# Optimization experiments

Measured on AMD Instinct MI355X. Metric: run time of the kernel, lower is better.

The kernel has to match this reference:

```python
import jax, jax.numpy as jnp
import numpy as np

D = 1024          # d_model
E = 12            # n_routed
HS = 2 * D        # shared hidden (r_shared=2)
HR = 3 * D        # routed hidden (r_routed=3)
TAU = 1.5         # router temperature


def setup_inputs() -> dict:
    key = jax.random.key(0)
    ks = jax.random.split(key, 12)
    def xavier(k, shape):
        fan_in, fan_out = shape[-2], shape[-1]
        lim = jnp.sqrt(6.0 / (fan_in + fan_out))
        return jax.random.uniform(k, shape, jnp.float32, -lim, lim)
    x = jax.random.normal(ks[0], (2, 1024, D), jnp.float32)
    # shared expert (n_shared=1, GEGLU)
    Ws1 = xavier(ks[1], (D, 2 * HS)); bs1 = jnp.zeros((2 * HS,), jnp.float32)
    Ws2 = xavier(ks[2], (HS, D));     bs2 = jnp.zeros((D,), jnp.float32)
    # routed experts, stacked [E, ...]
    We1 = xavier(ks[3], (E, D, 2 * HR)); be1 = jnp.zeros((E, 2 * HR), jnp.float32)
    We2 = xavier(ks[4], (E, HR, D));     be2 = jnp.zeros((E, D), jnp.float32)
    # router
    Wr = xavier(ks[5], (D, E)); br = jnp.zeros((E,), jnp.float32)
    return {"x": x, "Ws1": Ws1, "bs1": bs1, "Ws2": Ws2, "bs2": bs2,
            "We1": We1, "be1": be1, "We2": We2, "be2": be2, "Wr": Wr, "br": br}


def _geglu(h):
    a, g = jnp.split(h, 2, axis=-1)
    return a * jax.nn.gelu(g, approximate=False)  # torch GELU is exact erf


def reference(x, Ws1, bs1, Ws2, bs2, We1, be1, We2, be2, Wr, br):
    B, T, Dm = x.shape
    xf = x.reshape(-1, Dm)                                   # [N, D]
    # shared expert (n_shared=1 -> divide by 1)
    ys = _geglu(xf @ Ws1 + bs1) @ Ws2 + bs2                  # [N, D]
    # top-2 router (eval: no noise)
    logits = (xf @ Wr + br) / TAU                            # [N, E]
    top_val, top_idx = jax.lax.top_k(logits, 2)              # [N, 2]
    top_w = jax.nn.softmax(top_val, axis=-1)                 # [N, 2]
    # combine weights per (token, expert); non-selected experts get 0
    onehot = jax.nn.one_hot(top_idx, E, dtype=x.dtype)       # [N, 2, E]
    w = jnp.einsum('nke,nk->ne', onehot, top_w)              # [N, E]
    # dropless dense dispatch: every expert sees all tokens, weight 0 masks
    h = jnp.einsum('nd,edh->enh', xf, We1) + be1[:, None, :] # [E, N, 2*HR]
    act = _geglu(h)                                          # [E, N, HR]
    yE = jnp.einsum('enh,ehd->end', act, We2) + be2[:, None, :]
    yr = jnp.einsum('end,ne->nd', yE, w)                     # [N, D]
    return (ys + yr).reshape(B, T, Dm)
```

## Files before the change

kernel.cpp:

```cpp
#include <hip/hip_runtime.h>

#define N_TOK 2048
#define DMODEL 1024
#define NEXP 12
#define HS_DIM 2048
#define HR_DIM 3072

typedef __attribute__((ext_vector_type(8))) short bf16x8;
typedef __attribute__((ext_vector_type(4))) float f32x4;

#define AS1 __attribute__((address_space(1)))
#define AS3 __attribute__((address_space(3)))

__device__ __forceinline__ void gl_lds16(const void* g, void* l) {
  __builtin_amdgcn_global_load_lds((const AS1 void*)g, (AS3 void*)l, 16, 0, 0);
}

__device__ __forceinline__ unsigned short f2bf(float x) {
  union { float f; unsigned int u; } v; v.f = x;
  unsigned int u = v.u;
  u += 0x7fff + ((u >> 16) & 1);
  return (unsigned short)(u >> 16);
}
__device__ __forceinline__ unsigned pack2(float a, float b) {
  return (unsigned)f2bf(a) | ((unsigned)f2bf(b) << 16);
}
__device__ __forceinline__ float gelu_exact(float x) {
  return 0.5f * x * (1.0f + erff(x * 0.70710678118654752f));
}


__global__ __launch_bounds__(256)
void convert_x_kernel(const float* __restrict__ X, unsigned short* __restrict__ XB) {
  const int idx = (blockIdx.x * 256 + threadIdx.x) * 8;
  float4 f0 = *(const float4*)(X + idx);
  float4 f1 = *(const float4*)(X + idx + 4);
  uint4 o;
  o.x = pack2(f0.x, f0.y); o.y = pack2(f0.z, f0.w);
  o.z = pack2(f1.x, f1.y); o.w = pack2(f1.z, f1.w);
  *(uint4*)(XB + idx) = o;
}

__global__ __launch_bounds__(256)
void tconv_kernel(const float* __restrict__ W, unsigned short* __restrict__ WT,
                  int K, int N) {
  const int n0 = blockIdx.x * 64;
  const int k0 = blockIdx.y * 64;
  const size_t bo = (size_t)blockIdx.z * K * N;
  __shared__ unsigned short Ts[64 * 72];
  const int t = threadIdx.x;
  const int k4 = (t >> 4) * 4, n4 = (t & 15) * 4;
  float4 rw[4];
#pragma unroll
  for (int i = 0; i < 4; ++i)
    rw[i] = *(const float4*)(W + bo + (size_t)(k0 + k4 + i) * N + n0 + n4);
#pragma unroll
  for (int j = 0; j < 4; ++j) {
    uint2 v;
    v.x = pack2(((const float*)&rw[0])[j], ((const float*)&rw[1])[j]);
    v.y = pack2(((const float*)&rw[2])[j], ((const float*)&rw[3])[j]);
    *(uint2*)&Ts[(n4 + j) * 72 + k4] = v;
  }
  __syncthreads();
  const int n = t >> 2, kc = (t & 3) * 16;
  uint4 v0 = *(const uint4*)&Ts[n * 72 + kc];
  uint4 v1 = *(const uint4*)&Ts[n * 72 + kc + 8];
  unsigned short* dst = WT + (size_t)blockIdx.z * N * K + (size_t)(n0 + n) * K + k0 + kc;
  *(uint4*)dst = v0;
  *(uint4*)(dst + 8) = v1;
}


__global__ void init_kernel(int* counts, int* cursors) {
  int t = threadIdx.x;
  if (t < NEXP) { counts[t] = 0; cursors[t] = 0; }
}

__global__ __launch_bounds__(256)
void router_kernel(const float* __restrict__ X, const float* __restrict__ Wr,
                   const float* __restrict__ br, int* __restrict__ top_e,
                   float* __restrict__ top_w, int* __restrict__ counts) {
  const int wv = threadIdx.x >> 6, lane = threadIdx.x & 63;
  const int n = blockIdx.x * 4 + wv;
  float a[NEXP];
#pragma unroll
  for (int e = 0; e < NEXP; ++e) a[e] = 0.f;
  for (int it = 0; it < DMODEL / 64; ++it) {
    int k = it * 64 + lane;
    float xv = X[(size_t)n * DMODEL + k];
    const float* wr = Wr + (size_t)k * NEXP;
#pragma unroll
    for (int e = 0; e < NEXP; ++e) a[e] += xv * wr[e];
  }
#pragma unroll
  for (int e = 0; e < NEXP; ++e)
    for (int o = 32; o > 0; o >>= 1) a[e] += __shfl_xor(a[e], o, 64);
  if (lane == 0) {
    float l[NEXP];
#pragma unroll
    for (int e = 0; e < NEXP; ++e) l[e] = (a[e] + br[e]) * (1.0f / 1.5f);
    int e0 = 0;
    for (int e = 1; e < NEXP; ++e) if (l[e] > l[e0]) e0 = e;
    int e1 = (e0 == 0) ? 1 : 0;
    for (int e = 0; e < NEXP; ++e) if (e != e0 && l[e] > l[e1]) e1 = e;
    float w0 = 1.f / (1.f + expf(l[e1] - l[e0]));
    top_e[n * 2 + 0] = e0; top_e[n * 2 + 1] = e1;
    top_w[n * 2 + 0] = w0; top_w[n * 2 + 1] = 1.f - w0;
    atomicAdd(&counts[e0], 1); atomicAdd(&counts[e1], 1);
  }
}

__global__ void scan_kernel(const int* __restrict__ counts, int* __restrict__ offs) {
  if (threadIdx.x == 0) {
    int s = 0;
    for (int e = 0; e < NEXP; ++e) { offs[e] = s; s += counts[e]; }
    offs[NEXP] = s;
  }
}

__global__ __launch_bounds__(256)
void fill_kernel(const int* __restrict__ top_e, const float* __restrict__ top_w,
                 const int* __restrict__ offs, int* __restrict__ cursors,
                 int* __restrict__ slot_tok, float* __restrict__ slot_w) {
  int n = blockIdx.x * 256 + threadIdx.x;
  if (n >= N_TOK) return;
#pragma unroll
  for (int j = 0; j < 2; ++j) {
    int e = top_e[n * 2 + j];
    int p = atomicAdd(&cursors[e], 1);
    int s = offs[e] + p;
    slot_tok[s] = n;
    slot_w[s] = top_w[n * 2 + j];
  }
}

__global__ __launch_bounds__(256, 2)
void gemm1_kernel(const unsigned short* __restrict__ XB,
                  const unsigned short* __restrict__ W1T,
                  const float* __restrict__ B1, unsigned short* __restrict__ ACT,
                  const int* __restrict__ slot_tok, const int* __restrict__ offs,
                  const int* __restrict__ counts, int H, int Mtot) {
  const int e = blockIdx.z;
  const int n0 = blockIdx.x * 128;
  const int m0 = blockIdx.y * 128;
  const int count = counts ? counts[e] : N_TOK;
  if (m0 >= count) return;
  const int off = offs ? offs[e] : 0;
  const unsigned short* W = W1T + (size_t)e * 2 * H * DMODEL;
  const float* bias = B1 + (size_t)e * 2 * H;

  __shared__ unsigned short As[128 * 32];
  __shared__ unsigned short Bs[256 * 32];

  const int t = threadIdx.x;
  const int lane = t & 63, wv = t >> 6;
  const int srow = t >> 2, skc = t & 3;

  int r0 = m0 + srow, r1 = m0 + srow + 64;
  if (slot_tok) {
    int s0 = off + r0; if (s0 >= Mtot) s0 = Mtot - 1;
    int s1 = off + r1; if (s1 >= Mtot) s1 = Mtot - 1;
    r0 = slot_tok[s0]; r1 = slot_tok[s1];
  }
  const unsigned short* ap0 = XB + (size_t)r0 * DMODEL + skc * 8;
  const unsigned short* ap1 = XB + (size_t)r1 * DMODEL + skc * 8;
  const unsigned short* bp[4];
#pragma unroll
  for (int ii = 0; ii < 4; ++ii) {
    int brow = srow + 64 * ii;
    int wrow = (brow < 128) ? (n0 + brow) : (H + n0 + brow - 128);
    bp[ii] = W + (size_t)wrow * DMODEL + skc * 8;
  }
  unsigned short* aL0 = &As[wv * 512];
  unsigned short* aL1 = &As[2048 + wv * 512];
  unsigned short* bL0 = &Bs[wv * 512];
  unsigned short* bL1 = &Bs[2048 + wv * 512];
  unsigned short* bL2 = &Bs[4096 + wv * 512];
  unsigned short* bL3 = &Bs[6144 + wv * 512];

  const int q = lane >> 4, rr = lane & 15;
  const int wr = wv >> 1, wc = wv & 1;

  f32x4 acc_a[4][4], acc_g[4][4];
#pragma unroll
  for (int i = 0; i < 4; ++i)
#pragma unroll
    for (int j = 0; j < 4; ++j) {
      acc_a[i][j] = (f32x4){0.f, 0.f, 0.f, 0.f};
      acc_g[i][j] = (f32x4){0.f, 0.f, 0.f, 0.f};
    }

  for (int kt = 0; kt < DMODEL / 32; ++kt) {
    const int kb = kt * 32;
    __syncthreads();
    gl_lds16(ap0 + kb, aL0);
    gl_lds16(ap1 + kb, aL1);
    gl_lds16(bp[0] + kb, bL0);
    gl_lds16(bp[1] + kb, bL1);
    gl_lds16(bp[2] + kb, bL2);
    gl_lds16(bp[3] + kb, bL3);
    __syncthreads();
    bf16x8 aF[4], bA[4], bG[4];
#pragma unroll
    for (int i = 0; i < 4; ++i)
      aF[i] = *(const bf16x8*)&As[(wr * 64 + i * 16 + rr) * 32 + q * 8];
#pragma unroll
    for (int j = 0; j < 4; ++j) {
      bA[j] = *(const bf16x8*)&Bs[(wc * 64 + j * 16 + rr) * 32 + q * 8];
      bG[j] = *(const bf16x8*)&Bs[(128 + wc * 64 + j * 16 + rr) * 32 + q * 8];
    }
#pragma unroll
    for (int i = 0; i < 4; ++i)
#pragma unroll
      for (int j = 0; j < 4; ++j) {
        acc_a[i][j] = __builtin_amdgcn_mfma_f32_16x16x32_bf16(aF[i], bA[j], acc_a[i][j], 0, 0, 0);
        acc_g[i][j] = __builtin_amdgcn_mfma_f32_16x16x32_bf16(aF[i], bG[j], acc_g[i][j], 0, 0, 0);
      }
  }

  float ba[4], bg[4];
#pragma unroll
  for (int j = 0; j < 4; ++j) {
    int col = wc * 64 + j * 16 + rr;
    ba[j] = bias[n0 + col];
    bg[j] = bias[H + n0 + col];
  }
#pragma unroll
  for (int i = 0; i < 4; ++i)
#pragma unroll
    for (int j = 0; j < 4; ++j)
#pragma unroll
      for (int reg = 0; reg < 4; ++reg) {
        int row = wr * 64 + i * 16 + q * 4 + reg;
        if (m0 + row < count) {
          int col = wc * 64 + j * 16 + rr;
          float av = acc_a[i][j][reg] + ba[j];
          float gv = acc_g[i][j][reg] + bg[j];
          ACT[(size_t)(off + m0 + row) * H + n0 + col] = f2bf(av * gelu_exact(gv));
        }
      }
}

__global__ __launch_bounds__(256, 2)
void gemm2_kernel(const unsigned short* __restrict__ ACT,
                  const unsigned short* __restrict__ W2T,
                  const float* __restrict__ B2, float* __restrict__ OUT,
                  const int* __restrict__ slot_tok, const float* __restrict__ slot_w,
                  const int* __restrict__ offs, const int* __restrict__ counts,
                  int K, int Mtot) {
  const int e = blockIdx.z;
  const int n0 = blockIdx.x * 128;
  const int m0 = blockIdx.y * 128;
  const int count = counts ? counts[e] : N_TOK;
  if (m0 >= count) return;
  const int off = offs ? offs[e] : 0;
  const unsigned short* W = W2T + (size_t)e * DMODEL * K;
  const float* bias = B2 + (size_t)e * DMODEL;

  __shared__ unsigned short As[128 * 32];
  __shared__ unsigned short Bs[128 * 32];

  const int t = threadIdx.x;
  const int lane = t & 63, wv = t >> 6;
  const int srow = t >> 2, skc = t & 3;

  int s0 = off + m0 + srow;      if (s0 >= Mtot) s0 = Mtot - 1;
  int s1 = off + m0 + srow + 64; if (s1 >= Mtot) s1 = Mtot - 1;
  const unsigned short* ap0 = ACT + (size_t)s0 * K + skc * 8;
  const unsigned short* ap1 = ACT + (size_t)s1 * K + skc * 8;
  const unsigned short* bp0 = W + (size_t)(n0 + srow) * K + skc * 8;
  const unsigned short* bp1 = W + (size_t)(n0 + srow + 64) * K + skc * 8;

  unsigned short* aL0 = &As[wv * 512];
  unsigned short* aL1 = &As[2048 + wv * 512];
  unsigned short* bL0 = &Bs[wv * 512];
  unsigned short* bL1 = &Bs[2048 + wv * 512];

  const int q = lane >> 4, rr = lane & 15;
  const int wr = wv >> 1, wc = wv & 1;

  f32x4 acc[4][4];
#pragma unroll
  for (int i = 0; i < 4; ++i)
#pragma unroll
    for (int j = 0; j < 4; ++j) acc[i][j] = (f32x4){0.f, 0.f, 0.f, 0.f};

  const int KT = K >> 5;
  for (int kt = 0; kt < KT; ++kt) {
    const int kb = kt * 32;
    __syncthreads();
    gl_lds16(ap0 + kb, aL0);
    gl_lds16(ap1 + kb, aL1);
    gl_lds16(bp0 + kb, bL0);
    gl_lds16(bp1 + kb, bL1);
    __syncthreads();
    bf16x8 aF[4], bF[4];
#pragma unroll
    for (int i = 0; i < 4; ++i)
      aF[i] = *(const bf16x8*)&As[(wr * 64 + i * 16 + rr) * 32 + q * 8];
#pragma unroll
    for (int j = 0; j < 4; ++j)
      bF[j] = *(const bf16x8*)&Bs[(wc * 64 + j * 16 + rr) * 32 + q * 8];
#pragma unroll
    for (int i = 0; i < 4; ++i)
#pragma unroll
      for (int j = 0; j < 4; ++j)
        acc[i][j] = __builtin_amdgcn_mfma_f32_16x16x32_bf16(aF[i], bF[j], acc[i][j], 0, 0, 0);
  }

  float bb[4];
#pragma unroll
  for (int j = 0; j < 4; ++j) bb[j] = bias[n0 + wc * 64 + j * 16 + rr];
#pragma unroll
  for (int i = 0; i < 4; ++i)
#pragma unroll
    for (int j = 0; j < 4; ++j)
#pragma unroll
      for (int reg = 0; reg < 4; ++reg) {
        int row = wr * 64 + i * 16 + q * 4 + reg;
        if (m0 + row < count) {
          int col = wc * 64 + j * 16 + rr;
          float v = acc[i][j][reg] + bb[j];
          if (slot_tok) {
            int s = off + m0 + row;
            atomicAdd(&OUT[(size_t)slot_tok[s] * DMODEL + n0 + col], slot_w[s] * v);
          } else {
            OUT[(size_t)(m0 + row) * DMODEL + n0 + col] = v;
          }
        }
      }
}


extern "C" void kernel_launch(void* const* d_in, const int* in_sizes, int n_in,
                              void* d_out, int out_size, void* d_ws, size_t ws_size,
                              hipStream_t stream) {
  const float* x   = (const float*)d_in[0];
  const float* Ws1 = (const float*)d_in[1];
  const float* bs1 = (const float*)d_in[2];
  const float* Ws2 = (const float*)d_in[3];
  const float* bs2 = (const float*)d_in[4];
  const float* We1 = (const float*)d_in[5];
  const float* be1 = (const float*)d_in[6];
  const float* We2 = (const float*)d_in[7];
  const float* be2 = (const float*)d_in[8];
  const float* Wr  = (const float*)d_in[9];
  const float* br  = (const float*)d_in[10];
  float* out = (float*)d_out;

  char* p = (char*)d_ws;
  int* counts  = (int*)p; p += 256;
  int* cursors = (int*)p; p += 256;
  int* offs    = (int*)p; p += 256;
  int* top_e   = (int*)p; p += (size_t)N_TOK * 2 * 4;
  float* top_w = (float*)p; p += (size_t)N_TOK * 2 * 4;
  int* slot_tok = (int*)p; p += (size_t)2 * N_TOK * 4;
  float* slot_w = (float*)p; p += (size_t)2 * N_TOK * 4;
  unsigned short* xb    = (unsigned short*)p; p += (size_t)N_TOK * DMODEL * 2;
  unsigned short* ws1t  = (unsigned short*)p; p += (size_t)2 * HS_DIM * DMODEL * 2;
  unsigned short* ws2t  = (unsigned short*)p; p += (size_t)DMODEL * HS_DIM * 2;
  unsigned short* we1t  = (unsigned short*)p; p += (size_t)NEXP * 2 * HR_DIM * DMODEL * 2;
  unsigned short* we2t  = (unsigned short*)p; p += (size_t)NEXP * DMODEL * HR_DIM * 2;
  unsigned short* act_s = (unsigned short*)p; p += (size_t)N_TOK * HS_DIM * 2;
  unsigned short* act_r = (unsigned short*)p; p += (size_t)2 * N_TOK * HR_DIM * 2;

  init_kernel<<<1, 64, 0, stream>>>(counts, cursors);
  router_kernel<<<N_TOK / 4, 256, 0, stream>>>(x, Wr, br, top_e, top_w, counts);
  scan_kernel<<<1, 64, 0, stream>>>(counts, offs);
  fill_kernel<<<N_TOK / 256, 256, 0, stream>>>(top_e, top_w, offs, cursors, slot_tok, slot_w);

  convert_x_kernel<<<(N_TOK * DMODEL) / 2048, 256, 0, stream>>>(x, xb);
  tconv_kernel<<<dim3(2 * HS_DIM / 64, DMODEL / 64, 1), 256, 0, stream>>>(Ws1, ws1t, DMODEL, 2 * HS_DIM);
  tconv_kernel<<<dim3(DMODEL / 64, HS_DIM / 64, 1), 256, 0, stream>>>(Ws2, ws2t, HS_DIM, DMODEL);
  tconv_kernel<<<dim3(2 * HR_DIM / 64, DMODEL / 64, NEXP), 256, 0, stream>>>(We1, we1t, DMODEL, 2 * HR_DIM);
  tconv_kernel<<<dim3(DMODEL / 64, HR_DIM / 64, NEXP), 256, 0, stream>>>(We2, we2t, HR_DIM, DMODEL);

  gemm1_kernel<<<dim3(HS_DIM / 128, N_TOK / 128, 1), 256, 0, stream>>>(
      xb, ws1t, bs1, act_s, nullptr, nullptr, nullptr, HS_DIM, N_TOK);
  gemm1_kernel<<<dim3(HR_DIM / 128, N_TOK / 128, NEXP), 256, 0, stream>>>(
      xb, we1t, be1, act_r, slot_tok, offs, counts, HR_DIM, 2 * N_TOK);

  gemm2_kernel<<<dim3(DMODEL / 128, N_TOK / 128, 1), 256, 0, stream>>>(
      act_s, ws2t, bs2, out, nullptr, nullptr, nullptr, nullptr, HS_DIM, N_TOK);
  gemm2_kernel<<<dim3(DMODEL / 128, N_TOK / 128, NEXP), 256, 0, stream>>>(
      act_r, we2t, be2, out, slot_tok, slot_w, offs, counts, HR_DIM, 2 * N_TOK);
}
```

Measured before the change: 1.030 ms.

## Merge shared and routed GEMMs into single launches with 32x32 MFMA and K=64 tiles

Combines the shared-expert and routed-expert GEMMs into one flat-grid launch per stage, so both sets of blocks can be scheduled together instead of running as separate serialized kernels. The compute moves from 16x16x32 to 32x32x16 bf16 MFMA and each K step loads 64 elements, which halves the number of barriers per tile and changes how fragments are reused. The output is now zeroed up front and the shared-expert result is written with atomics, which adds a zeroing pass and atomic traffic for the shared path. LDS use per block doubles, which may lower occupancy.

```diff
diff --git a/kernel.cpp b/kernel.cpp
--- a/kernel.cpp
+++ b/kernel.cpp
@@ -7,7 +7,7 @@
 #define HR_DIM 3072
 
 typedef __attribute__((ext_vector_type(8))) short bf16x8;
-typedef __attribute__((ext_vector_type(4))) float f32x4;
+typedef __attribute__((ext_vector_type(16))) float f32x16;
 
 #define AS1 __attribute__((address_space(1)))
 #define AS3 __attribute__((address_space(3)))
@@ -47,7 +47,7 @@
   const int n0 = blockIdx.x * 64;
   const int k0 = blockIdx.y * 64;
   const size_t bo = (size_t)blockIdx.z * K * N;
-  __shared__ unsigned short Ts[64 * 72];
+  __shared__ __align__(16) unsigned short Ts[64 * 72];
   const int t = threadIdx.x;
   const int k4 = (t >> 4) * 4, n4 = (t & 15) * 4;
   float4 rw[4];
@@ -134,198 +134,243 @@
   }
 }
 
+__global__ __launch_bounds__(256)
+void zero_out_kernel(float4* __restrict__ out) {
+  out[blockIdx.x * 256 + threadIdx.x] = make_float4(0.f, 0.f, 0.f, 0.f);
+}
+
+#define G1_SHARED 256
+#define G1_PER_E  384
+
 __global__ __launch_bounds__(256, 2)
-void gemm1_kernel(const unsigned short* __restrict__ XB,
-                  const unsigned short* __restrict__ W1T,
-                  const float* __restrict__ B1, unsigned short* __restrict__ ACT,
-                  const int* __restrict__ slot_tok, const int* __restrict__ offs,
-                  const int* __restrict__ counts, int H, int Mtot) {
-  const int e = blockIdx.z;
-  const int n0 = blockIdx.x * 128;
-  const int m0 = blockIdx.y * 128;
-  const int count = counts ? counts[e] : N_TOK;
+void gemm1_all_kernel(const unsigned short* __restrict__ XB,
+                      const unsigned short* __restrict__ WS,
+                      const unsigned short* __restrict__ WE,
+                      const float* __restrict__ BSb, const float* __restrict__ BEb,
+                      unsigned short* __restrict__ ACT_S, unsigned short* __restrict__ ACT_R,
+                      const int* __restrict__ slot_tok, const int* __restrict__ offs,
+                      const int* __restrict__ counts) {
+  int id = blockIdx.x;
+  const unsigned short* W; const float* bias; unsigned short* ACT;
+  int H, count, off, m0, n0, routed;
+  if (id < G1_SHARED) {
+    routed = 0;
+    m0 = (id >> 4) * 128; n0 = (id & 15) * 128;
+    W = WS; bias = BSb; ACT = ACT_S; H = HS_DIM; count = N_TOK; off = 0;
+  } else {
+    routed = 1;
+    id -= G1_SHARED;
+    const int e = id / G1_PER_E, rem = id % G1_PER_E;
+    m0 = (rem / 24) * 128; n0 = (rem % 24) * 128;
+    W = WE + (size_t)e * 2 * HR_DIM * DMODEL;
+    bias = BEb + (size_t)e * 2 * HR_DIM;
+    ACT = ACT_R; H = HR_DIM; count = counts[e]; off = offs[e];
+  }
   if (m0 >= count) return;
-  const int off = offs ? offs[e] : 0;
-  const unsigned short* W = W1T + (size_t)e * 2 * H * DMODEL;
-  const float* bias = B1 + (size_t)e * 2 * H;
-
-  __shared__ unsigned short As[128 * 32];
-  __shared__ unsigned short Bs[256 * 32];
+
+  __shared__ __align__(16) unsigned short As[2 * 4096];
+  __shared__ __align__(16) unsigned short Bs[2 * 8192];
 
   const int t = threadIdx.x;
   const int lane = t & 63, wv = t >> 6;
   const int srow = t >> 2, skc = t & 3;
-
-  int r0 = m0 + srow, r1 = m0 + srow + 64;
-  if (slot_tok) {
-    int s0 = off + r0; if (s0 >= Mtot) s0 = Mtot - 1;
-    int s1 = off + r1; if (s1 >= Mtot) s1 = Mtot - 1;
-    r0 = slot_tok[s0]; r1 = slot_tok[s1];
-  }
-  const unsigned short* ap0 = XB + (size_t)r0 * DMODEL + skc * 8;
-  const unsigned short* ap1 = XB + (size_t)r1 * DMODEL + skc * 8;
+  const int ln31 = lane & 31, hi = lane >> 5;
+  const int wr = wv >> 1, wc = wv & 1;
+
+  const unsigned short* ap[2];
+#pragma unroll
+  for (int g = 0; g < 2; ++g) {
+    int mr = m0 + srow + 64 * g;
+    int tok;
+    if (routed) {
+      int s = off + (mr < count ? mr : count - 1);
+      tok = slot_tok[s];
+    } else {
+      tok = mr;
+    }
+    ap[g] = XB + (size_t)tok * DMODEL + skc * 8;
+  }
   const unsigned short* bp[4];
 #pragma unroll
-  for (int ii = 0; ii < 4; ++ii) {
-    int brow = srow + 64 * ii;
+  for (int g = 0; g < 4; ++g) {
+    int brow = srow + 64 * g;
     int wrow = (brow < 128) ? (n0 + brow) : (H + n0 + brow - 128);
-    bp[ii] = W + (size_t)wrow * DMODEL + skc * 8;
-  }
-  unsigned short* aL0 = &As[wv * 512];
-  unsigned short* aL1 = &As[2048 + wv * 512];
-  unsigned short* bL0 = &Bs[wv * 512];
-  unsigned short* bL1 = &Bs[2048 + wv * 512];
-  unsigned short* bL2 = &Bs[4096 + wv * 512];
-  unsigned short* bL3 = &Bs[6144 + wv * 512];
-
-  const int q = lane >> 4, rr = lane & 15;
-  const int wr = wv >> 1, wc = wv & 1;
-
-  f32x4 acc_a[4][4], acc_g[4][4];
-#pragma unroll
-  for (int i = 0; i < 4; ++i)
-#pragma unroll
-    for (int j = 0; j < 4; ++j) {
-      acc_a[i][j] = (f32x4){0.f, 0.f, 0.f, 0.f};
-      acc_g[i][j] = (f32x4){0.f, 0.f, 0.f, 0.f};
+    bp[g] = W + (size_t)wrow * DMODEL + skc * 8;
+  }
+
+  f32x16 acc_a[2][2], acc_g[2][2];
+  const f32x16 z16 = {0.f,0.f,0.f,0.f,0.f,0.f,0.f,0.f,0.f,0.f,0.f,0.f,0.f,0.f,0.f,0.f};
+#pragma unroll
+  for (int i = 0; i < 2; ++i)
+#pragma unroll
+    for (int j = 0; j < 2; ++j) { acc_a[i][j] = z16; acc_g[i][j] = z16; }
+
+  for (int kt = 0; kt < DMODEL / 64; ++kt) {
+    const int kb = kt * 64;
+    __syncthreads();
+#pragma unroll
+    for (int h = 0; h < 2; ++h) {
+#pragma unroll
+      for (int g = 0; g < 2; ++g)
+        gl_lds16(ap[g] + kb + h * 32, &As[h * 4096 + g * 2048 + wv * 512]);
+#pragma unroll
+      for (int g = 0; g < 4; ++g)
+        gl_lds16(bp[g] + kb + h * 32, &Bs[h * 8192 + g * 2048 + wv * 512]);
     }
-
-  for (int kt = 0; kt < DMODEL / 32; ++kt) {
-    const int kb = kt * 32;
     __syncthreads();
-    gl_lds16(ap0 + kb, aL0);
-    gl_lds16(ap1 + kb, aL1);
-    gl_lds16(bp[0] + kb, bL0);
-    gl_lds16(bp[1] + kb, bL1);
-    gl_lds16(bp[2] + kb, bL2);
-    gl_lds16(bp[3] + kb, bL3);
-    __syncthreads();
-    bf16x8 aF[4], bA[4], bG[4];
-#pragma unroll
-    for (int i = 0; i < 4; ++i)
-      aF[i] = *(const bf16x8*)&As[(wr * 64 + i * 16 + rr) * 32 + q * 8];
-#pragma unroll
-    for (int j = 0; j < 4; ++j) {
-      bA[j] = *(const bf16x8*)&Bs[(wc * 64 + j * 16 + rr) * 32 + q * 8];
-      bG[j] = *(const bf16x8*)&Bs[(128 + wc * 64 + j * 16 + rr) * 32 + q * 8];
+#pragma unroll
+    for (int ks = 0; ks < 4; ++ks) {
+      const int h = ks >> 1;
+      const int ko = (ks & 1) * 16 + hi * 8;
+      bf16x8 aF[2], bA[2], bG[2];
+#pragma unroll
+      for (int i = 0; i < 2; ++i)
+        aF[i] = *(const bf16x8*)&As[h * 4096 + (wr * 64 + i * 32 + ln31) * 32 + ko];
+#pragma unroll
+      for (int j = 0; j < 2; ++j) {
+        bA[j] = *(const bf16x8*)&Bs[h * 8192 + (wc * 64 + j * 32 + ln31) * 32 + ko];
+        bG[j] = *(const bf16x8*)&Bs[h * 8192 + (128 + wc * 64 + j * 32 + ln31) * 32 + ko];
+      }
+#pragma unroll
+      for (int i = 0; i < 2; ++i)
+#pragma unroll
+        for (int j = 0; j < 2; ++j) {
+          acc_a[i][j] = __builtin_amdgcn_mfma_f32_32x32x16_bf16(aF[i], bA[j], acc_a[i][j], 0, 0, 0);
+          acc_g[i][j] = __builtin_amdgcn_mfma_f32_32x32x16_bf16(aF[i], bG[j], acc_g[i][j], 0, 0, 0);
+        }
     }
-#pragma unroll
-    for (int i = 0; i < 4; ++i)
-#pragma unroll
-      for (int j = 0; j < 4; ++j) {
-        acc_a[i][j] = __builtin_amdgcn_mfma_f32_16x16x32_bf16(aF[i], bA[j], acc_a[i][j], 0, 0, 0);
-        acc_g[i][j] = __builtin_amdgcn_mfma_f32_16x16x32_bf16(aF[i], bG[j], acc_g[i][j], 0, 0, 0);
-      }
-  }
-
-  float ba[4], bg[4];
-#pragma unroll
-  for (int j = 0; j < 4; ++j) {
-    int col = wc * 64 + j * 16 + rr;
-    ba[j] = bias[n0 + col];
-    bg[j] = bias[H + n0 + col];
-  }
-#pragma unroll
-  for (int i = 0; i < 4; ++i)
-#pragma unroll
-    for (int j = 0; j < 4; ++j)
-#pragma unroll
-      for (int reg = 0; reg < 4; ++reg) {
-        int row = wr * 64 + i * 16 + q * 4 + reg;
+  }
+
+  float ba[2], bg[2];
+#pragma unroll
+  for (int j = 0; j < 2; ++j) {
+    int col = n0 + wc * 64 + j * 32 + ln31;
+    ba[j] = bias[col];
+    bg[j] = bias[H + col];
+  }
+#pragma unroll
+  for (int i = 0; i < 2; ++i)
+#pragma unroll
+    for (int j = 0; j < 2; ++j)
+#pragma unroll
+      for (int reg = 0; reg < 16; ++reg) {
+        int row = wr * 64 + i * 32 + (reg & 3) + 8 * (reg >> 2) + 4 * hi;
         if (m0 + row < count) {
-          int col = wc * 64 + j * 16 + rr;
+          int col = n0 + wc * 64 + j * 32 + ln31;
           float av = acc_a[i][j][reg] + ba[j];
           float gv = acc_g[i][j][reg] + bg[j];
-          ACT[(size_t)(off + m0 + row) * H + n0 + col] = f2bf(av * gelu_exact(gv));
+          ACT[(size_t)(off + m0 + row) * H + col] = f2bf(av * gelu_exact(gv));
         }
       }
 }
 
+#define G2_SHARED 128
+#define G2_PER_E  128
+
 __global__ __launch_bounds__(256, 2)
-void gemm2_kernel(const unsigned short* __restrict__ ACT,
-                  const unsigned short* __restrict__ W2T,
-                  const float* __restrict__ B2, float* __restrict__ OUT,
-                  const int* __restrict__ slot_tok, const float* __restrict__ slot_w,
-                  const int* __restrict__ offs, const int* __restrict__ counts,
-                  int K, int Mtot) {
-  const int e = blockIdx.z;
-  const int n0 = blockIdx.x * 128;
-  const int m0 = blockIdx.y * 128;
-  const int count = counts ? counts[e] : N_TOK;
+void gemm2_all_kernel(const unsigned short* __restrict__ ACT_S,
+                      const unsigned short* __restrict__ ACT_R,
+                      const unsigned short* __restrict__ WSt,
+                      const unsigned short* __restrict__ WEt,
+                      const float* __restrict__ BSb, const float* __restrict__ BEb,
+                      float* __restrict__ OUT,
+                      const int* __restrict__ slot_tok, const float* __restrict__ slot_w,
+                      const int* __restrict__ offs, const int* __restrict__ counts) {
+  int id = blockIdx.x;
+  const unsigned short* A; const unsigned short* W; const float* bias;
+  int K, count, off, m0, n0, routed;
+  if (id < G2_SHARED) {
+    routed = 0;
+    m0 = (id >> 3) * 128; n0 = (id & 7) * 128;
+    A = ACT_S; W = WSt; bias = BSb; K = HS_DIM; count = N_TOK; off = 0;
+  } else {
+    routed = 1;
+    id -= G2_SHARED;
+    const int e = id / G2_PER_E, rem = id % G2_PER_E;
+    m0 = (rem >> 3) * 128; n0 = (rem & 7) * 128;
+    A = ACT_R; W = WEt + (size_t)e * DMODEL * HR_DIM;
+    bias = BEb + (size_t)e * DMODEL; K = HR_DIM; count = counts[e]; off = offs[e];
+  }
   if (m0 >= count) return;
-  const int off = offs ? offs[e] : 0;
-  const unsigned short* W = W2T + (size_t)e * DMODEL * K;
-  const float* bias = B2 + (size_t)e * DMODEL;
-
-  __shared__ unsigned short As[128 * 32];
-  __shared__ unsigned short Bs[128 * 32];
+
+  __shared__ __align__(16) unsigned short As[2 * 4096];
+  __shared__ __align__(16) unsigned short Bs[2 * 4096];
 
   const int t = threadIdx.x;
   const int lane = t & 63, wv = t >> 6;
   const int srow = t >> 2, skc = t & 3;
-
-  int s0 = off + m0 + srow;      if (s0 >= Mtot) s0 = Mtot - 1;
-  int s1 = off + m0 + srow + 64; if (s1 >= Mtot) s1 = Mtot - 1;
-  const unsigned short* ap0 = ACT + (size_t)s0 * K + skc * 8;
-  const unsigned short* ap1 = ACT + (size_t)s1 * K + skc * 8;
-  const unsigned short* bp0 = W + (size_t)(n0 + srow) * K + skc * 8;
-  const unsigned short* bp1 = W + (size_t)(n0 + srow + 64) * K + skc * 8;
-
-  unsigned short* aL0 = &As[wv * 512];
-  unsigned short* aL1 = &As[2048 + wv * 512];
-  unsigned short* bL0 = &Bs[wv * 512];
-  unsigned short* bL1 = &Bs[2048 + wv * 512];
-
-  const int q = lane >> 4, rr = lane & 15;
+  const int ln31 = lane & 31, hi = lane >> 5;
   const int wr = wv >> 1, wc = wv & 1;
 
-  f32x4 acc[4][4];
-#pragma unroll
-  for (int i = 0; i < 4; ++i)
-#pragma unroll
-    for (int j = 0; j < 4; ++j) acc[i][j] = (f32x4){0.f, 0.f, 0.f, 0.f};
-
-  const int KT = K >> 5;
+  const unsigned short* ap[2];
+#pragma unroll
+  for (int g = 0; g < 2; ++g) {
+    int mr = m0 + srow + 64 * g;
+    int r = off + (mr < count ? mr : count - 1);
+    ap[g] = A + (size_t)r * K + skc * 8;
+  }
+  const unsigned short* bp[2];
+#pragma unroll
+  for (int g = 0; g < 2; ++g)
+    bp[g] = W + (size_t)(n0 + srow + 64 * g) * K + skc * 8;
+
+  f32x16 acc[2][2];
+  const f32x16 z16 = {0.f,0.f,0.f,0.f,0.f,0.f,0.f,0.f,0.f,0.f,0.f,0.f,0.f,0.f,0.f,0.f};
+#pragma unroll
+  for (int i = 0; i < 2; ++i)
+#pragma unroll
+    for (int j = 0; j < 2; ++j) acc[i][j] = z16;
+
+  const int KT = K >> 6;
   for (int kt = 0; kt < KT; ++kt) {
-    const int kb = kt * 32;
+    const int kb = kt * 64;
     __syncthreads();
-    gl_lds16(ap0 + kb, aL0);
-    gl_lds16(ap1 + kb, aL1);
-    gl_lds16(bp0 + kb, bL0);
-    gl_lds16(bp1 + kb, bL1);
+#pragma unroll
+    for (int h = 0; h < 2; ++h) {
+#pragma unroll
+      for (int g = 0; g < 2; ++g) {
+        gl_lds16(ap[g] + kb + h * 32, &As[h * 4096 + g * 2048 + wv * 512]);
+        gl_lds16(bp[g] + kb + h * 32, &Bs[h * 4096 + g * 2048 + wv * 512]);
+      }
+    }
     __syncthreads();
-    bf16x8 aF[4], bF[4];
-#pragma unroll
-    for (int i = 0; i < 4; ++i)
-      aF[i] = *(const bf16x8*)&As[(wr * 64 + i * 16 + rr) * 32 + q * 8];
-#pragma unroll
-    for (int j = 0; j < 4; ++j)
-      bF[j] = *(const bf16x8*)&Bs[(wc * 64 + j * 16 + rr) * 32 + q * 8];
-#pragma unroll
-    for (int i = 0; i < 4; ++i)
-#pragma unroll
-      for (int j = 0; j < 4; ++j)
-        acc[i][j] = __builtin_amdgcn_mfma_f32_16x16x32_bf16(aF[i], bF[j], acc[i][j], 0, 0, 0);
-  }
-
-  float bb[4];
-#pragma unroll
-  for (int j = 0; j < 4; ++j) bb[j] = bias[n0 + wc * 64 + j * 16 + rr];
-#pragma unroll
-  for (int i = 0; i < 4; ++i)
-#pragma unroll
-    for (int j = 0; j < 4; ++j)
-#pragma unroll
-      for (int reg = 0; reg < 4; ++reg) {
-        int row = wr * 64 + i * 16 + q * 4 + reg;
+#pragma unroll
+    for (int ks = 0; ks < 4; ++ks) {
+      const int h = ks >> 1;
+      const int ko = (ks & 1) * 16 + hi * 8;
+      bf16x8 aF[2], bF[2];
+#pragma unroll
+      for (int i = 0; i < 2; ++i)
+        aF[i] = *(const bf16x8*)&As[h * 4096 + (wr * 64 + i * 32 + ln31) * 32 + ko];
+#pragma unroll
+      for (int j = 0; j < 2; ++j)
+        bF[j] = *(const bf16x8*)&Bs[h * 4096 + (wc * 64 + j * 32 + ln31) * 32 + ko];
+#pragma unroll
+      for (int i = 0; i < 2; ++i)
+#pragma unroll
+        for (int j = 0; j < 2; ++j)
+          acc[i][j] = __builtin_amdgcn_mfma_f32_32x32x16_bf16(aF[i], bF[j], acc[i][j], 0, 0, 0);
+    }
+  }
+
+  float bb[2];
+#pragma unroll
+  for (int j = 0; j < 2; ++j) bb[j] = bias[n0 + wc * 64 + j * 32 + ln31];
+#pragma unroll
+  for (int i = 0; i < 2; ++i)
+#pragma unroll
+    for (int j = 0; j < 2; ++j)
+#pragma unroll
+      for (int reg = 0; reg < 16; ++reg) {
+        int row = wr * 64 + i * 32 + (reg & 3) + 8 * (reg >> 2) + 4 * hi;
         if (m0 + row < count) {
-          int col = wc * 64 + j * 16 + rr;
+          int col = n0 + wc * 64 + j * 32 + ln31;
           float v = acc[i][j][reg] + bb[j];
-          if (slot_tok) {
+          if (routed) {
             int s = off + m0 + row;
-            atomicAdd(&OUT[(size_t)slot_tok[s] * DMODEL + n0 + col], slot_w[s] * v);
+            atomicAdd(&OUT[(size_t)slot_tok[s] * DMODEL + col], slot_w[s] * v);
           } else {
-            OUT[(size_t)(m0 + row) * DMODEL + n0 + col] = v;
+            atomicAdd(&OUT[(size_t)(m0 + row) * DMODEL + col], v);
           }
         }
       }
@@ -364,10 +409,7 @@
   unsigned short* act_s = (unsigned short*)p; p += (size_t)N_TOK * HS_DIM * 2;
   unsigned short* act_r = (unsigned short*)p; p += (size_t)2 * N_TOK * HR_DIM * 2;
 
-  init_kernel<<<1, 64, 0, stream>>>(counts, cursors);
-  router_kernel<<<N_TOK / 4, 256, 0, stream>>>(x, Wr, br, top_e, top_w, counts);
-  scan_kernel<<<1, 64, 0, stream>>>(counts, offs);
-  fill_kernel<<<N_TOK / 256, 256, 0, stream>>>(top_e, top_w, offs, cursors, slot_tok, slot_w);
+  zero_out_kernel<<<(N_TOK * DMODEL) / 1024, 256, 0, stream>>>((float4*)out);
 
   convert_x_kernel<<<(N_TOK * DMODEL) / 2048, 256, 0, stream>>>(x, xb);
   tconv_kernel<<<dim3(2 * HS_DIM / 64, DMODEL / 64, 1), 256, 0, stream>>>(Ws1, ws1t, DMODEL, 2 * HS_DIM);
@@ -375,13 +417,14 @@
   tconv_kernel<<<dim3(2 * HR_DIM / 64, DMODEL / 64, NEXP), 256, 0, stream>>>(We1, we1t, DMODEL, 2 * HR_DIM);
   tconv_kernel<<<dim3(DMODEL / 64, HR_DIM / 64, NEXP), 256, 0, stream>>>(We2, we2t, HR_DIM, DMODEL);
 
-  gemm1_kernel<<<dim3(HS_DIM / 128, N_TOK / 128, 1), 256, 0, stream>>>(
-      xb, ws1t, bs1, act_s, nullptr, nullptr, nullptr, HS_DIM, N_TOK);
-  gemm1_kernel<<<dim3(HR_DIM / 128, N_TOK / 128, NEXP), 256, 0, stream>>>(
-      xb, we1t, be1, act_r, slot_tok, offs, counts, HR_DIM, 2 * N_TOK);
-
-  gemm2_kernel<<<dim3(DMODEL / 128, N_TOK / 128, 1), 256, 0, stream>>>(
-      act_s, ws2t, bs2, out, nullptr, nullptr, nullptr, nullptr, HS_DIM, N_TOK);
-  gemm2_kernel<<<dim3(DMODEL / 128, N_TOK / 128, NEXP), 256, 0, stream>>>(
-      act_r, we2t, be2, out, slot_tok, slot_w, offs, counts, HR_DIM, 2 * N_TOK);
-}
+  init_kernel<<<1, 64, 0, stream>>>(counts, cursors);
+  router_kernel<<<N_TOK / 4, 256, 0, stream>>>(x, Wr, br, top_e, top_w, counts);
+  scan_kernel<<<1, 64, 0, stream>>>(counts, offs);
+  fill_kernel<<<N_TOK / 256, 256, 0, stream>>>(top_e, top_w, offs, cursors, slot_tok, slot_w);
+
+  gemm1_all_kernel<<<G1_SHARED + G1_PER_E * NEXP, 256, 0, stream>>>(
+      xb, ws1t, we1t, bs1, be1, act_s, act_r, slot_tok, offs, counts);
+
+  gemm2_all_kernel<<<G2_SHARED + G2_PER_E * NEXP, 256, 0, stream>>>(
+      act_s, act_r, ws2t, we2t, bs2, be2, out, slot_tok, slot_w, offs, counts);
+}
```

After: 967.6 us. -6.1%, faster.
